# Optimization experiments

Hardware: AMD Instinct MI355X
Metric: run time of the kernel (lower is better)

## Reference

```python
import jax, jax.numpy as jnp
import numpy as np

TOP_K = 2


def setup_inputs() -> dict:
    key = jax.random.key(0)
    ks = jax.random.split(key, 6)
    B, S, H, I, E = 4, 2048, 1024, 4096, 8
    x = jax.random.normal(ks[0], (B, S, H), dtype=jnp.float32)
    Wr = jax.random.normal(ks[1], (H, E), dtype=jnp.float32) * (1.0 / np.sqrt(H))
    W1 = jax.random.normal(ks[2], (E, H, I), dtype=jnp.float32) * (1.0 / np.sqrt(H))
    b1 = jnp.zeros((E, I), dtype=jnp.float32)
    W2 = jax.random.normal(ks[3], (E, I, H), dtype=jnp.float32) * (1.0 / np.sqrt(I))
    b2 = jnp.zeros((E, H), dtype=jnp.float32)
    return {"x": x, "Wr": Wr, "W1": W1, "b1": b1, "W2": W2, "b2": b2}


def reference(x, Wr, W1, b1, W2, b2):
    B, S, H = x.shape
    E = Wr.shape[1]
    xf = x.reshape(-1, H)                              # [T, H], T = B*S
    logits = xf @ Wr                                   # [T, E]
    probs = jax.nn.softmax(logits, axis=-1)
    rw, sel = jax.lax.top_k(probs, TOP_K)              # [T, K]
    rw = rw / jnp.sum(rw, axis=-1, keepdims=True)
    out = jnp.zeros_like(xf)
    # Loop over small fixed expert count; each token contributes only via its
    # top-k combine weight (zero weight == not routed, matching index_add).
    for i in range(E):
        wi = jnp.sum(jnp.where(sel == i, rw, 0.0), axis=-1)    # [T]
        h = jax.nn.silu(xf @ W1[i] + b1[i])                    # [T, I]
        out = out + (h @ W2[i] + b2[i]) * wi[:, None]
    return out.reshape(B, S, H)
```

## Files before the change

kernel.cpp:

```cpp
#include <hip/hip_runtime.h>
#include <cstdint>
#include <cstddef>

#define TTOK 8192
#define HDIM 1024
#define IDIM 4096
#define NEXP 8
#define PMAX 18432
#define WS_NEED 302260352ULL

#define SLOT 32768

typedef __attribute__((ext_vector_type(8))) short bf16x8;
typedef __attribute__((ext_vector_type(4))) float f32x4;

#define AS3 __attribute__((address_space(3)))
#define AS1 __attribute__((address_space(1)))

__device__ __forceinline__ void gld16(const void* g, void* s) {
  __builtin_amdgcn_global_load_lds((const AS1 void*)g, (AS3 void*)s, 16, 0, 0);
}

__device__ __forceinline__ unsigned short f2b(float f) {
  unsigned u = __builtin_bit_cast(unsigned, f);
  unsigned r = ((u >> 16) & 1u) + 0x7FFFu;
  return (unsigned short)((u + r) >> 16);
}

__global__ __launch_bounds__(256, 2) void router_k(
    const float* __restrict__ x, const float* __restrict__ wr,
    unsigned short* __restrict__ xb, int* __restrict__ t2e,
    float* __restrict__ t2w)
{
  const int t = blockIdx.x * 4 + (threadIdx.x >> 6);
  const int l = threadIdx.x & 63;
  const float* xr = x + (size_t)t * HDIM;
  float acc[8] = {0.f,0.f,0.f,0.f,0.f,0.f,0.f,0.f};
  #pragma unroll
  for (int j = 0; j < 4; ++j) {
    const int base = j * 256 + l * 4;
    const float4 xv = *(const float4*)(xr + base);
    const float xa[4] = {xv.x, xv.y, xv.z, xv.w};
    ushort4 ub;
    ub.x = f2b(xa[0]); ub.y = f2b(xa[1]); ub.z = f2b(xa[2]); ub.w = f2b(xa[3]);
    *(ushort4*)(xb + (size_t)t * HDIM + base) = ub;
    #pragma unroll
    for (int ii = 0; ii < 4; ++ii) {
      const float4 w0 = *(const float4*)(wr + (size_t)(base + ii) * 8);
      const float4 w1 = *(const float4*)(wr + (size_t)(base + ii) * 8 + 4);
      acc[0] += xa[ii] * w0.x; acc[1] += xa[ii] * w0.y;
      acc[2] += xa[ii] * w0.z; acc[3] += xa[ii] * w0.w;
      acc[4] += xa[ii] * w1.x; acc[5] += xa[ii] * w1.y;
      acc[6] += xa[ii] * w1.z; acc[7] += xa[ii] * w1.w;
    }
  }
  #pragma unroll
  for (int e = 0; e < 8; ++e) {
    float v = acc[e];
    #pragma unroll
    for (int off = 32; off > 0; off >>= 1) v += __shfl_xor(v, off);
    acc[e] = v;
  }
  if (l == 0) {
    float l0 = -1e30f; int i0 = 0;
    #pragma unroll
    for (int e = 0; e < 8; ++e) if (acc[e] > l0) { l0 = acc[e]; i0 = e; }
    float l1 = -1e30f; int i1 = (i0 == 0) ? 1 : 0;
    #pragma unroll
    for (int e = 0; e < 8; ++e) if (e != i0 && acc[e] > l1) { l1 = acc[e]; i1 = e; }
    const float w0 = 1.f / (1.f + expf(l1 - l0));
    t2e[t * 2] = i0; t2e[t * 2 + 1] = i1;
    t2w[t * 2] = w0; t2w[t * 2 + 1] = 1.f - w0;
  }
}

__global__ void count_k(const int* __restrict__ t2e, int* __restrict__ meta) {
  const int t = threadIdx.x, w = t >> 6, l = t & 63;
  int cnt[8] = {0,0,0,0,0,0,0,0};
  for (int c = 0; c < 16; ++c) {
    const int tok = (w * 16 + c) * 64 + l;
    const int e0 = t2e[2 * tok], e1 = t2e[2 * tok + 1];
    #pragma unroll
    for (int e = 0; e < 8; ++e)
      cnt[e] += __popcll(__ballot(e0 == e)) + __popcll(__ballot(e1 == e));
  }
  __shared__ int part[8][8];
  if (l == 0) {
    #pragma unroll
    for (int e = 0; e < 8; ++e) part[w][e] = cnt[e];
  }
  __syncthreads();
  if (t == 0) {
    int off = 0;
    #pragma unroll
    for (int e = 0; e < 8; ++e) {
      int s = 0;
      #pragma unroll
      for (int w2 = 0; w2 < 8; ++w2) s += part[w2][e];
      meta[e] = s; meta[16 + e] = off; off += (s + 255) & ~255;
    }
    meta[24] = off;
  }
}

__global__ void scatter_k(const int* __restrict__ t2e, const int* __restrict__ meta,
                          int* __restrict__ ltok, int* __restrict__ t2p)
{
  const int e = blockIdx.x;
  const int t = threadIdx.x, w = t >> 6, l = t & 63;
  const int off = meta[16 + e];
  const int cnt = meta[e];
  __shared__ int wsum[4];
  __shared__ int base;
  if (t == 0) base = 0;
  __syncthreads();
  const unsigned long long lt = (1ULL << l) - 1ULL;
  for (int c = 0; c < TTOK / 256; ++c) {
    const int tok = c * 256 + t;
    const bool m0 = (t2e[2 * tok] == e);
    const bool m1 = (t2e[2 * tok + 1] == e);
    const unsigned long long b0 = __ballot(m0);
    const unsigned long long b1 = __ballot(m1);
    const int n0 = __popcll(b0), n1 = __popcll(b1);
    const int r0 = __popcll(b0 & lt);
    const int r1 = n0 + __popcll(b1 & lt);
    if (l == 0) wsum[w] = n0 + n1;
    __syncthreads();
    int wb = base;
    #pragma unroll
    for (int i = 0; i < 4; ++i) if (i < w) wb += wsum[i];
    const int tot = wsum[0] + wsum[1] + wsum[2] + wsum[3];
    __syncthreads();
    if (t == 0) base += tot;
    if (m0) { const int p = off + wb + r0; ltok[p] = tok; t2p[2 * tok] = p; }
    if (m1) { const int p = off + wb + r1; ltok[p] = tok; t2p[2 * tok + 1] = p; }
    __syncthreads();
  }
  const int padded = (cnt + 255) & ~255;
  for (int i = cnt + t; i < padded; i += 256) ltok[off + i] = -1;
}

__global__ __launch_bounds__(256, 2) void packT_k(const float* __restrict__ src,
                                                  unsigned short* __restrict__ dst,
                                                  int K, int N)
{
  const int tiles_n = N >> 8, tiles_k = K >> 5;
  const int bid = blockIdx.x;
  const int e = bid / (tiles_k * tiles_n);
  const int rem = bid % (tiles_k * tiles_n);
  const int kt = rem / tiles_n, it = rem % tiles_n;
  const float* S = src + (size_t)e * K * N + (size_t)kt * 32 * N + (size_t)it * 256;
  unsigned short* D = dst + (size_t)e * N * K + (size_t)it * 256 * K + (size_t)kt * 32;
  __shared__ uint32_t lds[256 * 17];
  const int t = threadIdx.x;
  #pragma unroll
  for (int q = 0; q < 4; ++q) {
    const int task = q * 256 + t;
    const int i4 = task & 63, kp = task >> 6;
    const float* p0 = S + (size_t)(2 * kp) * N + i4 * 4;
    const float4 r0 = *(const float4*)p0;
    const float4 r1 = *(const float4*)(p0 + N);
    const float a0[4] = {r0.x, r0.y, r0.z, r0.w};
    const float a1[4] = {r1.x, r1.y, r1.z, r1.w};
    #pragma unroll
    for (int j = 0; j < 4; ++j)
      lds[(i4 * 4 + j) * 17 + kp] = (uint32_t)f2b(a0[j]) | ((uint32_t)f2b(a1[j]) << 16);
  }
  __syncthreads();
  #pragma unroll
  for (int r = 0; r < 4; ++r) {
    const int idx = r * 256 + t;
    const int il = idx >> 2, q4 = idx & 3;
    uint4 o;
    o.x = lds[il * 17 + q4 * 4 + 0];
    o.y = lds[il * 17 + q4 * 4 + 1];
    o.z = lds[il * 17 + q4 * 4 + 2];
    o.w = lds[il * 17 + q4 * 4 + 3];
    *(uint4*)(D + (size_t)il * K + q4 * 8) = o;
  }
}


__global__ __launch_bounds__(512, 2) void gemm1_k(
    const unsigned short* __restrict__ xb, const unsigned short* __restrict__ w1t,
    const float* __restrict__ b1, const int* __restrict__ meta,
    const int* __restrict__ ltok, unsigned short* __restrict__ h)
{
  const int wg = blockIdx.x;
  const int id = (wg & 7) * (1152 / 8) + (wg >> 3);
  const int mt = id >> 4, nt = id & 15;
  if (mt * 256 >= meta[24]) return;
  int e = 0;
  #pragma unroll
  for (int i = 1; i < 8; ++i) if (meta[16 + i] <= mt * 256) e = i;

  extern __shared__ char lds[];
  const int t = threadIdx.x;
  const int w = t >> 6, l = t & 63;
  const int wa = w >> 2, wb = w & 3;

  const unsigned short* asrc[2]; const unsigned short* bsrc[2];
  #pragma unroll
  for (int c = 0; c < 2; ++c) {
    const int G = c * 512 + t;
    const int line = G >> 3, q = (G & 7) ^ (line & 7);
    const int row = 2 * line + (q >> 2), g = q & 3;
    asrc[c] = w1t + ((size_t)e * IDIM + nt * 256 + row) * HDIM + g * 8;
    int tok = ltok[mt * 256 + row]; if (tok < 0) tok = 0;
    bsrc[c] = xb + (size_t)tok * HDIM + g * 8;
  }

  const int lr = l & 15, lg = l >> 4;
  f32x4 acc[8][4] = {};

  auto STAGE_A = [&](int kt) {
    char* sb = lds + (kt % 3) * SLOT;
    const int ks = kt * 32;
    gld16(asrc[0] + ks, sb + w * 1024);
    gld16(asrc[1] + ks, sb + 8192 + w * 1024);
  };
  auto STAGE_B = [&](int kt) {
    char* sb = lds + (kt % 3) * SLOT + 16384;
    const int ks = kt * 32;
    gld16(bsrc[0] + ks, sb + w * 1024);
    gld16(bsrc[1] + ks, sb + 8192 + w * 1024);
  };

  STAGE_A(0); STAGE_B(0);
  STAGE_A(1); STAGE_B(1);
  const int NT = HDIM / 32;
  for (int kt = 0; kt < NT; ++kt) {
    const char* sl = lds + (kt % 3) * SLOT;
    if (kt + 2 < NT) {
      STAGE_A(kt + 2);
      asm volatile("s_waitcnt vmcnt(6)" ::: "memory");
    } else if (kt + 1 < NT) {
      asm volatile("s_waitcnt vmcnt(4)" ::: "memory");
    } else {
      asm volatile("s_waitcnt vmcnt(0)" ::: "memory");
    }
    __builtin_amdgcn_s_barrier();
    bf16x8 af[8];
    #pragma unroll
    for (int fm = 0; fm < 8; ++fm) {
      const int row = wa * 128 + fm * 16 + lr;
      const int line = row >> 1;
      const int p = (((row & 1) << 2) + lg) ^ (line & 7);
      af[fm] = *(const bf16x8*)(sl + line * 128 + p * 16);
    }
    bf16x8 bf01[2];
    #pragma unroll
    for (int fn = 0; fn < 2; ++fn) {
      const int row = wb * 64 + fn * 16 + lr;
      const int line = row >> 1;
      const int p = (((row & 1) << 2) + lg) ^ (line & 7);
      bf01[fn] = *(const bf16x8*)(sl + 16384 + line * 128 + p * 16);
    }
    __builtin_amdgcn_s_setprio(1);
    #pragma unroll
    for (int fm = 0; fm < 8; ++fm)
      #pragma unroll
      for (int fn = 0; fn < 2; ++fn)
        acc[fm][fn] = __builtin_amdgcn_mfma_f32_16x16x32_bf16(af[fm], bf01[fn], acc[fm][fn], 0, 0, 0);
    __builtin_amdgcn_s_setprio(0);
    __builtin_amdgcn_s_barrier();
    if (kt + 2 < NT) STAGE_B(kt + 2);
    __builtin_amdgcn_s_barrier();
    bf16x8 bf23[2];
    #pragma unroll
    for (int fn = 0; fn < 2; ++fn) {
      const int row = wb * 64 + (fn + 2) * 16 + lr;
      const int line = row >> 1;
      const int p = (((row & 1) << 2) + lg) ^ (line & 7);
      bf23[fn] = *(const bf16x8*)(sl + 16384 + line * 128 + p * 16);
    }
    __builtin_amdgcn_s_setprio(1);
    #pragma unroll
    for (int fm = 0; fm < 8; ++fm)
      #pragma unroll
      for (int fn = 0; fn < 2; ++fn)
        acc[fm][fn + 2] = __builtin_amdgcn_mfma_f32_16x16x32_bf16(af[fm], bf23[fn], acc[fm][fn + 2], 0, 0, 0);
    __builtin_amdgcn_s_setprio(0);
    __builtin_amdgcn_s_barrier();
  }

  const int lg4 = lg * 4;
  #pragma unroll
  for (int fm = 0; fm < 8; ++fm) {
    const int ib = nt * 256 + wa * 128 + fm * 16 + lg4;
    const float4 b1v = *(const float4*)(b1 + e * IDIM + ib);
    #pragma unroll
    for (int fn = 0; fn < 4; ++fn) {
      const int trow = mt * 256 + wb * 64 + fn * 16 + lr;
      const float v0 = acc[fm][fn][0] + b1v.x;
      const float v1 = acc[fm][fn][1] + b1v.y;
      const float v2 = acc[fm][fn][2] + b1v.z;
      const float v3 = acc[fm][fn][3] + b1v.w;
      ushort4 st;
      st.x = f2b(v0 / (1.f + __expf(-v0)));
      st.y = f2b(v1 / (1.f + __expf(-v1)));
      st.z = f2b(v2 / (1.f + __expf(-v2)));
      st.w = f2b(v3 / (1.f + __expf(-v3)));
      *(ushort4*)(h + (size_t)trow * IDIM + ib) = st;
    }
  }
}

__global__ __launch_bounds__(512, 2) void gemm2_k(
    const unsigned short* __restrict__ h, const unsigned short* __restrict__ w2t,
    const int* __restrict__ meta, float* __restrict__ y)
{
  const int wg = blockIdx.x;
  const int id = (wg & 7) * (288 / 8) + (wg >> 3);
  const int mt = id >> 2, nt = id & 3;
  if (mt * 256 >= meta[24]) return;
  int e = 0;
  #pragma unroll
  for (int i = 1; i < 8; ++i) if (meta[16 + i] <= mt * 256) e = i;

  extern __shared__ char lds[];
  const int t = threadIdx.x;
  const int w = t >> 6, l = t & 63;
  const int wa = w >> 2, wb = w & 3;

  const unsigned short* asrc[2]; const unsigned short* bsrc[2];
  #pragma unroll
  for (int c = 0; c < 2; ++c) {
    const int G = c * 512 + t;
    const int line = G >> 3, q = (G & 7) ^ (line & 7);
    const int row = 2 * line + (q >> 2), g = q & 3;
    asrc[c] = w2t + ((size_t)e * HDIM + nt * 256 + row) * IDIM + g * 8;
    bsrc[c] = h + (size_t)(mt * 256 + row) * IDIM + g * 8;
  }

  const int lr = l & 15, lg = l >> 4;
  f32x4 acc[8][4] = {};

  auto STAGE_A = [&](int kt) {
    char* sb = lds + (kt % 3) * SLOT;
    const int ks = kt * 32;
    gld16(asrc[0] + ks, sb + w * 1024);
    gld16(asrc[1] + ks, sb + 8192 + w * 1024);
  };
  auto STAGE_B = [&](int kt) {
    char* sb = lds + (kt % 3) * SLOT + 16384;
    const int ks = kt * 32;
    gld16(bsrc[0] + ks, sb + w * 1024);
    gld16(bsrc[1] + ks, sb + 8192 + w * 1024);
  };

  STAGE_A(0); STAGE_B(0);
  STAGE_A(1); STAGE_B(1);
  const int NT = IDIM / 32;
  for (int kt = 0; kt < NT; ++kt) {
    const char* sl = lds + (kt % 3) * SLOT;
    if (kt + 2 < NT) {
      STAGE_A(kt + 2);
      asm volatile("s_waitcnt vmcnt(6)" ::: "memory");
    } else if (kt + 1 < NT) {
      asm volatile("s_waitcnt vmcnt(4)" ::: "memory");
    } else {
      asm volatile("s_waitcnt vmcnt(0)" ::: "memory");
    }
    __builtin_amdgcn_s_barrier();
    bf16x8 af[8];
    #pragma unroll
    for (int fm = 0; fm < 8; ++fm) {
      const int row = wa * 128 + fm * 16 + lr;
      const int line = row >> 1;
      const int p = (((row & 1) << 2) + lg) ^ (line & 7);
      af[fm] = *(const bf16x8*)(sl + line * 128 + p * 16);
    }
    bf16x8 bf01[2];
    #pragma unroll
    for (int fn = 0; fn < 2; ++fn) {
      const int row = wb * 64 + fn * 16 + lr;
      const int line = row >> 1;
      const int p = (((row & 1) << 2) + lg) ^ (line & 7);
      bf01[fn] = *(const bf16x8*)(sl + 16384 + line * 128 + p * 16);
    }
    __builtin_amdgcn_s_setprio(1);
    #pragma unroll
    for (int fm = 0; fm < 8; ++fm)
      #pragma unroll
      for (int fn = 0; fn < 2; ++fn)
        acc[fm][fn] = __builtin_amdgcn_mfma_f32_16x16x32_bf16(af[fm], bf01[fn], acc[fm][fn], 0, 0, 0);
    __builtin_amdgcn_s_setprio(0);
    __builtin_amdgcn_s_barrier();
    if (kt + 2 < NT) STAGE_B(kt + 2);
    __builtin_amdgcn_s_barrier();
    bf16x8 bf23[2];
    #pragma unroll
    for (int fn = 0; fn < 2; ++fn) {
      const int row = wb * 64 + (fn + 2) * 16 + lr;
      const int line = row >> 1;
      const int p = (((row & 1) << 2) + lg) ^ (line & 7);
      bf23[fn] = *(const bf16x8*)(sl + 16384 + line * 128 + p * 16);
    }
    __builtin_amdgcn_s_setprio(1);
    #pragma unroll
    for (int fm = 0; fm < 8; ++fm)
      #pragma unroll
      for (int fn = 0; fn < 2; ++fn)
        acc[fm][fn + 2] = __builtin_amdgcn_mfma_f32_16x16x32_bf16(af[fm], bf23[fn], acc[fm][fn + 2], 0, 0, 0);
    __builtin_amdgcn_s_setprio(0);
    __builtin_amdgcn_s_barrier();
  }

  const int lg4 = lg * 4;
  #pragma unroll
  for (int fm = 0; fm < 8; ++fm) {
    const int colb = nt * 256 + wa * 128 + fm * 16 + lg4;
    #pragma unroll
    for (int fn = 0; fn < 4; ++fn) {
      const int row = mt * 256 + wb * 64 + fn * 16 + lr;
      float4 st;
      st.x = acc[fm][fn][0]; st.y = acc[fm][fn][1];
      st.z = acc[fm][fn][2]; st.w = acc[fm][fn][3];
      *(float4*)(y + (size_t)row * HDIM + colb) = st;
    }
  }
}

__global__ __launch_bounds__(256, 4) void combine_k(
    const float* __restrict__ y, const float* __restrict__ b2,
    const int* __restrict__ t2e, const float* __restrict__ t2w,
    const int* __restrict__ t2p, float* __restrict__ out)
{
  const int t = blockIdx.x * 4 + (threadIdx.x >> 6);
  const int l = threadIdx.x & 63;
  const int e0 = t2e[t * 2], e1 = t2e[t * 2 + 1];
  const float w0 = t2w[t * 2], w1v = t2w[t * 2 + 1];
  const int p0 = t2p[t * 2], p1 = t2p[t * 2 + 1];
  const float* y0 = y + (size_t)p0 * HDIM;
  const float* y1 = y + (size_t)p1 * HDIM;
  const float* bb0 = b2 + e0 * HDIM;
  const float* bb1 = b2 + e1 * HDIM;
  float* o = out + (size_t)t * HDIM;
  #pragma unroll
  for (int j = 0; j < 4; ++j) {
    const int c = j * 256 + l * 4;
    const float4 a = *(const float4*)(y0 + c);
    const float4 b = *(const float4*)(y1 + c);
    const float4 c0 = *(const float4*)(bb0 + c);
    const float4 c1 = *(const float4*)(bb1 + c);
    float4 r;
    r.x = w0 * (a.x + c0.x) + w1v * (b.x + c1.x);
    r.y = w0 * (a.y + c0.y) + w1v * (b.y + c1.y);
    r.z = w0 * (a.z + c0.z) + w1v * (b.z + c1.z);
    r.w = w0 * (a.w + c0.w) + w1v * (b.w + c1.w);
    *(float4*)(o + c) = r;
  }
}

__global__ void sentinel_k(float* out) { out[0] = 1.0e6f; }

extern "C" void kernel_launch(void* const* d_in, const int* in_sizes, int n_in,
                              void* d_out, int out_size, void* d_ws, size_t ws_size,
                              hipStream_t stream)
{
  (void)in_sizes; (void)n_in; (void)out_size;
  const float* x  = (const float*)d_in[0];
  const float* wr = (const float*)d_in[1];
  const float* w1 = (const float*)d_in[2];
  const float* b1 = (const float*)d_in[3];
  const float* w2 = (const float*)d_in[4];
  const float* b2 = (const float*)d_in[5];
  float* out = (float*)d_out;
  char* ws = (char*)d_ws;

  if (ws_size < WS_NEED) { sentinel_k<<<1, 1, 0, stream>>>(out); return; }

  unsigned short* xb  = (unsigned short*)(ws);
  unsigned short* w1t = (unsigned short*)(ws + 16777216);
  unsigned short* w2t = (unsigned short*)(ws + 83886080);
  unsigned short* h   = (unsigned short*)(ws + 150994944);
  int*   t2e  = (int*)(ws + 301989888);
  float* t2w  = (float*)(ws + 302055424);
  int*   ltok = (int*)(ws + 302120960);
  int*   t2p  = (int*)(ws + 302194688);
  int*   meta = (int*)(ws + 302260224);
  float* y    = (float*)(ws);

  hipFuncSetAttribute((const void*)gemm1_k, hipFuncAttributeMaxDynamicSharedMemorySize, 3 * SLOT);
  hipFuncSetAttribute((const void*)gemm2_k, hipFuncAttributeMaxDynamicSharedMemorySize, 3 * SLOT);

  router_k<<<TTOK / 4, 256, 0, stream>>>(x, wr, xb, t2e, t2w);
  packT_k<<<NEXP * (HDIM / 32) * (IDIM / 256), 256, 0, stream>>>(w1, w1t, HDIM, IDIM);
  packT_k<<<NEXP * (IDIM / 32) * (HDIM / 256), 256, 0, stream>>>(w2, w2t, IDIM, HDIM);
  count_k<<<1, 512, 0, stream>>>(t2e, meta);
  scatter_k<<<NEXP, 256, 0, stream>>>(t2e, meta, ltok, t2p);

  gemm1_k<<<72 * 16, 512, 3 * SLOT, stream>>>(xb, w1t, b1, meta, ltok, h);
  gemm2_k<<<72 * 4, 512, 3 * SLOT, stream>>>(h, w2t, meta, y);
  combine_k<<<TTOK / 4, 256, 0, stream>>>(y, b2, t2e, t2w, t2p, out);
}
```

Baseline: 572.7 us.

## Restructure GEMM pipelines into half-stage loads with pinned barriers

Both expert GEMM main loops now split each prefetch stage into two halves, each loading part of A and part of B, issued at two points per iteration. Scheduling barriers pin the s_barrier calls and explicit lgkmcnt waits. This aims to spread global-to-LDS traffic more evenly across the iteration and keep the compiler from moving LDS reads across barriers. It risks changing the vmcnt accounting and adds explicit waits that may serialize LDS reads with MFMA issue.

```diff
diff --git a/kernel.cpp b/kernel.cpp
--- a/kernel.cpp
+++ b/kernel.cpp
@@ -9,7 +9,7 @@
 #define PMAX 18432
 #define WS_NEED 302260352ULL
 
-#define SLOT 32768
+#define SLOTG 32768
 
 typedef __attribute__((ext_vector_type(8))) short bf16x8;
 typedef __attribute__((ext_vector_type(4))) float f32x4;
@@ -19,6 +19,17 @@
 
 __device__ __forceinline__ void gld16(const void* g, void* s) {
   __builtin_amdgcn_global_load_lds((const AS1 void*)g, (AS3 void*)s, 16, 0, 0);
+}
+
+__device__ __forceinline__ void pinned_barrier() {
+  __builtin_amdgcn_sched_barrier(0);
+  __builtin_amdgcn_s_barrier();
+  __builtin_amdgcn_sched_barrier(0);
+}
+
+__device__ __forceinline__ void wait_lds() {
+  asm volatile("s_waitcnt lgkmcnt(0)" ::: "memory");
+  __builtin_amdgcn_sched_barrier(0);
 }
 
 __device__ __forceinline__ unsigned short f2b(float f) {
@@ -213,34 +224,22 @@
   const int lr = l & 15, lg = l >> 4;
   f32x4 acc[8][4] = {};
 
-  auto STAGE_A = [&](int kt) {
-    char* sb = lds + (kt % 3) * SLOT;
+  auto STAGE_H = [&](int kt, int c) {
+    char* sb = lds + (kt % 3) * SLOTG;
     const int ks = kt * 32;
-    gld16(asrc[0] + ks, sb + w * 1024);
-    gld16(asrc[1] + ks, sb + 8192 + w * 1024);
+    gld16(asrc[c] + ks, sb + (c * 512 + w * 64) * 16);
+    gld16(bsrc[c] + ks, sb + 16384 + (c * 512 + w * 64) * 16);
   };
-  auto STAGE_B = [&](int kt) {
-    char* sb = lds + (kt % 3) * SLOT + 16384;
-    const int ks = kt * 32;
-    gld16(bsrc[0] + ks, sb + w * 1024);
-    gld16(bsrc[1] + ks, sb + 8192 + w * 1024);
-  };
-
-  STAGE_A(0); STAGE_B(0);
-  STAGE_A(1); STAGE_B(1);
+
+  STAGE_H(0, 0); STAGE_H(0, 1); STAGE_H(1, 0); STAGE_H(1, 1);
+  asm volatile("s_waitcnt vmcnt(4)" ::: "memory");
+  pinned_barrier();
+
   const int NT = HDIM / 32;
   for (int kt = 0; kt < NT; ++kt) {
-    const char* sl = lds + (kt % 3) * SLOT;
-    if (kt + 2 < NT) {
-      STAGE_A(kt + 2);
-      asm volatile("s_waitcnt vmcnt(6)" ::: "memory");
-    } else if (kt + 1 < NT) {
-      asm volatile("s_waitcnt vmcnt(4)" ::: "memory");
-    } else {
-      asm volatile("s_waitcnt vmcnt(0)" ::: "memory");
-    }
-    __builtin_amdgcn_s_barrier();
-    bf16x8 af[8];
+    const char* sl = lds + (kt % 3) * SLOTG;
+    const bool pf = (kt + 2 < NT);
+    bf16x8 af[8], b01[2];
     #pragma unroll
     for (int fm = 0; fm < 8; ++fm) {
       const int row = wa * 128 + fm * 16 + lr;
@@ -248,40 +247,48 @@
       const int p = (((row & 1) << 2) + lg) ^ (line & 7);
       af[fm] = *(const bf16x8*)(sl + line * 128 + p * 16);
     }
-    bf16x8 bf01[2];
     #pragma unroll
     for (int fn = 0; fn < 2; ++fn) {
       const int row = wb * 64 + fn * 16 + lr;
       const int line = row >> 1;
       const int p = (((row & 1) << 2) + lg) ^ (line & 7);
-      bf01[fn] = *(const bf16x8*)(sl + 16384 + line * 128 + p * 16);
-    }
+      b01[fn] = *(const bf16x8*)(sl + 16384 + line * 128 + p * 16);
+    }
+    if (pf) STAGE_H(kt + 2, 0);
+    pinned_barrier();
+    wait_lds();
     __builtin_amdgcn_s_setprio(1);
     #pragma unroll
     for (int fm = 0; fm < 8; ++fm)
       #pragma unroll
       for (int fn = 0; fn < 2; ++fn)
-        acc[fm][fn] = __builtin_amdgcn_mfma_f32_16x16x32_bf16(af[fm], bf01[fn], acc[fm][fn], 0, 0, 0);
+        acc[fm][fn] = __builtin_amdgcn_mfma_f32_16x16x32_bf16(af[fm], b01[fn], acc[fm][fn], 0, 0, 0);
     __builtin_amdgcn_s_setprio(0);
-    __builtin_amdgcn_s_barrier();
-    if (kt + 2 < NT) STAGE_B(kt + 2);
-    __builtin_amdgcn_s_barrier();
-    bf16x8 bf23[2];
+    pinned_barrier();
+    bf16x8 b23[2];
     #pragma unroll
     for (int fn = 0; fn < 2; ++fn) {
       const int row = wb * 64 + (fn + 2) * 16 + lr;
       const int line = row >> 1;
       const int p = (((row & 1) << 2) + lg) ^ (line & 7);
-      bf23[fn] = *(const bf16x8*)(sl + 16384 + line * 128 + p * 16);
-    }
+      b23[fn] = *(const bf16x8*)(sl + 16384 + line * 128 + p * 16);
+    }
+    if (pf) {
+      STAGE_H(kt + 2, 1);
+      asm volatile("s_waitcnt vmcnt(4)" ::: "memory");
+    } else if (kt + 1 < NT) {
+      asm volatile("s_waitcnt vmcnt(0)" ::: "memory");
+    }
+    pinned_barrier();
+    wait_lds();
     __builtin_amdgcn_s_setprio(1);
     #pragma unroll
     for (int fm = 0; fm < 8; ++fm)
       #pragma unroll
       for (int fn = 0; fn < 2; ++fn)
-        acc[fm][fn + 2] = __builtin_amdgcn_mfma_f32_16x16x32_bf16(af[fm], bf23[fn], acc[fm][fn + 2], 0, 0, 0);
+        acc[fm][fn + 2] = __builtin_amdgcn_mfma_f32_16x16x32_bf16(af[fm], b23[fn], acc[fm][fn + 2], 0, 0, 0);
     __builtin_amdgcn_s_setprio(0);
-    __builtin_amdgcn_s_barrier();
+    pinned_barrier();
   }
 
   const int lg4 = lg * 4;
@@ -336,34 +343,22 @@
   const int lr = l & 15, lg = l >> 4;
   f32x4 acc[8][4] = {};
 
-  auto STAGE_A = [&](int kt) {
-    char* sb = lds + (kt % 3) * SLOT;
+  auto STAGE_H = [&](int kt, int c) {
+    char* sb = lds + (kt % 3) * SLOTG;
     const int ks = kt * 32;
-    gld16(asrc[0] + ks, sb + w * 1024);
-    gld16(asrc[1] + ks, sb + 8192 + w * 1024);
+    gld16(asrc[c] + ks, sb + (c * 512 + w * 64) * 16);
+    gld16(bsrc[c] + ks, sb + 16384 + (c * 512 + w * 64) * 16);
   };
-  auto STAGE_B = [&](int kt) {
-    char* sb = lds + (kt % 3) * SLOT + 16384;
-    const int ks = kt * 32;
-    gld16(bsrc[0] + ks, sb + w * 1024);
-    gld16(bsrc[1] + ks, sb + 8192 + w * 1024);
-  };
-
-  STAGE_A(0); STAGE_B(0);
-  STAGE_A(1); STAGE_B(1);
+
+  STAGE_H(0, 0); STAGE_H(0, 1); STAGE_H(1, 0); STAGE_H(1, 1);
+  asm volatile("s_waitcnt vmcnt(4)" ::: "memory");
+  pinned_barrier();
+
   const int NT = IDIM / 32;
   for (int kt = 0; kt < NT; ++kt) {
-    const char* sl = lds + (kt % 3) * SLOT;
-    if (kt + 2 < NT) {
-      STAGE_A(kt + 2);
-      asm volatile("s_waitcnt vmcnt(6)" ::: "memory");
-    } else if (kt + 1 < NT) {
-      asm volatile("s_waitcnt vmcnt(4)" ::: "memory");
-    } else {
-      asm volatile("s_waitcnt vmcnt(0)" ::: "memory");
-    }
-    __builtin_amdgcn_s_barrier();
-    bf16x8 af[8];
+    const char* sl = lds + (kt % 3) * SLOTG;
+    const bool pf = (kt + 2 < NT);
+    bf16x8 af[8], b01[2];
     #pragma unroll
     for (int fm = 0; fm < 8; ++fm) {
       const int row = wa * 128 + fm * 16 + lr;
@@ -371,40 +366,48 @@
       const int p = (((row & 1) << 2) + lg) ^ (line & 7);
       af[fm] = *(const bf16x8*)(sl + line * 128 + p * 16);
     }
-    bf16x8 bf01[2];
     #pragma unroll
     for (int fn = 0; fn < 2; ++fn) {
       const int row = wb * 64 + fn * 16 + lr;
       const int line = row >> 1;
       const int p = (((row & 1) << 2) + lg) ^ (line & 7);
-      bf01[fn] = *(const bf16x8*)(sl + 16384 + line * 128 + p * 16);
-    }
+      b01[fn] = *(const bf16x8*)(sl + 16384 + line * 128 + p * 16);
+    }
+    if (pf) STAGE_H(kt + 2, 0);
+    pinned_barrier();
+    wait_lds();
     __builtin_amdgcn_s_setprio(1);
     #pragma unroll
     for (int fm = 0; fm < 8; ++fm)
       #pragma unroll
       for (int fn = 0; fn < 2; ++fn)
-        acc[fm][fn] = __builtin_amdgcn_mfma_f32_16x16x32_bf16(af[fm], bf01[fn], acc[fm][fn], 0, 0, 0);
+        acc[fm][fn] = __builtin_amdgcn_mfma_f32_16x16x32_bf16(af[fm], b01[fn], acc[fm][fn], 0, 0, 0);
     __builtin_amdgcn_s_setprio(0);
-    __builtin_amdgcn_s_barrier();
-    if (kt + 2 < NT) STAGE_B(kt + 2);
-    __builtin_amdgcn_s_barrier();
-    bf16x8 bf23[2];
+    pinned_barrier();
+    bf16x8 b23[2];
     #pragma unroll
     for (int fn = 0; fn < 2; ++fn) {
       const int row = wb * 64 + (fn + 2) * 16 + lr;
       const int line = row >> 1;
       const int p = (((row & 1) << 2) + lg) ^ (line & 7);
-      bf23[fn] = *(const bf16x8*)(sl + 16384 + line * 128 + p * 16);
-    }
+      b23[fn] = *(const bf16x8*)(sl + 16384 + line * 128 + p * 16);
+    }
+    if (pf) {
+      STAGE_H(kt + 2, 1);
+      asm volatile("s_waitcnt vmcnt(4)" ::: "memory");
+    } else if (kt + 1 < NT) {
+      asm volatile("s_waitcnt vmcnt(0)" ::: "memory");
+    }
+    pinned_barrier();
+    wait_lds();
     __builtin_amdgcn_s_setprio(1);
     #pragma unroll
     for (int fm = 0; fm < 8; ++fm)
       #pragma unroll
       for (int fn = 0; fn < 2; ++fn)
-        acc[fm][fn + 2] = __builtin_amdgcn_mfma_f32_16x16x32_bf16(af[fm], bf23[fn], acc[fm][fn + 2], 0, 0, 0);
+        acc[fm][fn + 2] = __builtin_amdgcn_mfma_f32_16x16x32_bf16(af[fm], b23[fn], acc[fm][fn + 2], 0, 0, 0);
     __builtin_amdgcn_s_setprio(0);
-    __builtin_amdgcn_s_barrier();
+    pinned_barrier();
   }
 
   const int lg4 = lg * 4;
@@ -482,8 +485,8 @@
   int*   meta = (int*)(ws + 302260224);
   float* y    = (float*)(ws);
 
-  hipFuncSetAttribute((const void*)gemm1_k, hipFuncAttributeMaxDynamicSharedMemorySize, 3 * SLOT);
-  hipFuncSetAttribute((const void*)gemm2_k, hipFuncAttributeMaxDynamicSharedMemorySize, 3 * SLOT);
+  hipFuncSetAttribute((const void*)gemm1_k, hipFuncAttributeMaxDynamicSharedMemorySize, 3 * SLOTG);
+  hipFuncSetAttribute((const void*)gemm2_k, hipFuncAttributeMaxDynamicSharedMemorySize, 3 * SLOTG);
 
   router_k<<<TTOK / 4, 256, 0, stream>>>(x, wr, xb, t2e, t2w);
   packT_k<<<NEXP * (HDIM / 32) * (IDIM / 256), 256, 0, stream>>>(w1, w1t, HDIM, IDIM);
@@ -491,7 +494,7 @@
   count_k<<<1, 512, 0, stream>>>(t2e, meta);
   scatter_k<<<NEXP, 256, 0, stream>>>(t2e, meta, ltok, t2p);
 
-  gemm1_k<<<72 * 16, 512, 3 * SLOT, stream>>>(xb, w1t, b1, meta, ltok, h);
-  gemm2_k<<<72 * 4, 512, 3 * SLOT, stream>>>(h, w2t, meta, y);
+  gemm1_k<<<72 * 16, 512, 3 * SLOTG, stream>>>(xb, w1t, b1, meta, ltok, h);
+  gemm2_k<<<72 * 4, 512, 3 * SLOTG, stream>>>(h, w2t, meta, y);
   combine_k<<<TTOK / 4, 256, 0, stream>>>(y, b2, t2e, t2w, t2p, out);
 }
```

After: 597.8 us. 1.04x slower.
